# Kernel optimization log

Hardware: AMD Instinct MI355X
Metric: run time of the kernel (lower is better)

The kernel has to match this reference:

```python
import jax, jax.numpy as jnp
import numpy as np

K = 3  # unfold kernel size
K2 = K * K


def conv1x1_relu(x, w):
    # x: (B, C, H, W), w: (O, C)  -- BasicConv2d(channel, channel, 1, bias=False) + ReLU
    return jax.nn.relu(jnp.einsum('bchw,oc->bohw', x, w))


def unfold3x3(x, d=1):
    # torch nn.Unfold(kernel_size=3, padding=d, dilation=d): returns (B, C, 9, H, W)
    # with kernel index k = 3*i + j varying per channel block (channel-major, matching
    # the '(c k2)' split in the original rearrange).
    B, C, H, W = x.shape
    xp = jnp.pad(x, ((0, 0), (0, 0), (d, d), (d, d)))
    pats = [xp[:, :, i * d:i * d + H, j * d:j * d + W]
            for i in range(K) for j in range(K)]
    return jnp.stack(pats, axis=2)  # (B, C, 9, H, W)


def setup_inputs() -> dict:
    key = jax.random.key(0)
    k0, k1, k2, k3 = jax.random.split(key, 4)
    n, t, c, h, w = 2, 4, 64, 64, 96
    x = jax.random.normal(k0, (n, t, c, h, w), dtype=jnp.float32)
    # BasicConv2d inits conv weights with std=0.01
    w1 = jax.random.normal(k1, (c, c), dtype=jnp.float32) * 0.01
    w2 = jax.random.normal(k2, (c, c), dtype=jnp.float32) * 0.01
    w3 = jax.random.normal(k3, (c, c), dtype=jnp.float32) * 0.01
    return {'x': x, 'w1': w1, 'w2': w2, 'w3': w3}


def reference(x, w1, w2, w3):
    n, t, c, h, w = x.shape
    hw = h * w
    xf = x.reshape(n * t, c, h, w)

    x1 = unfold3x3(conv1x1_relu(xf, w1))  # (nt, c, 9, h, w)
    x2 = unfold3x3(conv1x1_relu(xf, w2))
    x3 = unfold3x3(conv1x1_relu(xf, w3))

    # x1: '(n t) (c k2) hw -> n hw t k2 c'
    x1 = x1.reshape(n, t, c, K2, hw).transpose(0, 4, 1, 3, 2)  # (n, hw, t, k2, c)
    x1_mean = jnp.mean(x1, axis=3)                              # (n, hw, t, c)
    x1_var = jnp.var(x1, axis=3, ddof=1)                        # unbiased
    x1f = x1.reshape(n, hw, t * K2, c)

    # x2: '(n t) (c k2) hw -> n hw c t k2'
    x2 = x2.reshape(n, t, c, K2, hw).transpose(0, 4, 2, 1, 3)   # (n, hw, c, t, k2)
    x2_mean = jnp.mean(x2, axis=4)                              # (n, hw, c, t)
    x2_var = jnp.var(x2, axis=4, ddof=1)
    x2f = x2.reshape(n, hw, c, t * K2)

    score1 = jax.nn.softmax(jnp.matmul(x1f, x2f), axis=-1)       # (n, hw, t*k2, t*k2)
    score2 = jax.nn.softmax(jnp.matmul(x1_var, x2_var), axis=-1) # (n, hw, t, t)
    score3 = jax.nn.softmax(jnp.matmul(x1_mean, x2_mean), axis=-1)

    # x3: '(n t) (c k2) hw -> n hw t (k2 c)'
    x3 = x3.reshape(n, t, c, K2, hw).transpose(0, 4, 1, 3, 2)   # (n, hw, t, k2, c)
    x3tk = x3.reshape(n, hw, t, K2 * c)
    x4 = jnp.matmul(score3, x3tk) + jnp.matmul(score2, x3tk)     # (n, hw, t, k2*c)
    x4 = x4.reshape(n, hw, t, K2, c)

    x3f = x3.reshape(n, hw, t * K2, c)
    x5 = jnp.matmul(score1, x3f).reshape(n, hw, t, K2, c)

    x6 = x5 + x4                                                 # (n, hw, t, k2, c)
    center = x6[:, :, :, K2 // 2, :][..., None]                  # (n, hw, t, c, 1)
    score4 = jax.nn.softmax(jnp.matmul(x6, center), axis=-2)     # (n, hw, t, k2, 1)
    out = jnp.sum(x6 * score4, axis=-2)                          # (n, hw, t, c)

    # 'n (h w) t c -> n t c h w'
    out = out.reshape(n, h, w, t, c).transpose(0, 3, 4, 1, 2)
    return out
```

## Files before the change

### kernel.cpp

```cpp
#include <hip/hip_runtime.h>

#define HW 6144
#define HH 64
#define WWID 96

typedef __attribute__((ext_vector_type(8))) _Float16 half8;
typedef __attribute__((ext_vector_type(2))) _Float16 half2v;
typedef __attribute__((ext_vector_type(8))) unsigned short ushort8;
typedef __attribute__((ext_vector_type(4))) float floatx4;
typedef __attribute__((ext_vector_type(4))) uint uint4v;
typedef __attribute__((ext_vector_type(4))) int int4v;

static __device__ __forceinline__ ushort f2h(float x) {
  _Float16 h = (_Float16)x;
  return __builtin_bit_cast(ushort, h);
}
static __device__ __forceinline__ float h2f(ushort b) {
  return (float)__builtin_bit_cast(_Float16, b);
}
static __device__ __forceinline__ uint pk2h(float a, float b) {
  return __builtin_bit_cast(uint, __builtin_amdgcn_cvt_pkrtz(a, b));
}
static __device__ __forceinline__ float hdot2(uint a, uint b, float c) {
#if __has_builtin(__builtin_amdgcn_fdot2)
  return __builtin_amdgcn_fdot2(__builtin_bit_cast(half2v, a),
                                __builtin_bit_cast(half2v, b), c, false);
#else
  c = fmaf(h2f((ushort)a), h2f((ushort)b), c);
  return fmaf(h2f((ushort)(a >> 16)), h2f((ushort)(b >> 16)), c);
#endif
}
static __device__ __forceinline__ half2v h2shfl16(half2v v) {
  return __builtin_bit_cast(half2v,
      (uint)__shfl_xor((int)__builtin_bit_cast(uint, v), 16));
}

__global__ __launch_bounds__(256) void conv_mfma_kernel(
    const float* __restrict__ X, const float* __restrict__ W1,
    const float* __restrict__ W2, const float* __restrict__ W3,
    ushort* __restrict__ Y1, ushort* __restrict__ Y2, ushort* __restrict__ Y3) {
  __shared__ __align__(16) ushort Xt[32 * 72];
  const int tid = threadIdx.x;
  const int wid = tid >> 6, lane = tid & 63;
  const int b = blockIdx.x / 192;
  const int p0 = (blockIdx.x % 192) * 32;

  if (blockIdx.x == 0 && tid < 96) {
    int which = tid >> 5, i = tid & 31;
    ushort* Ys = which == 0 ? Y1 : which == 1 ? Y2 : Y3;
    ((uint*)(Ys + (size_t)8 * HW * 64))[i] = 0u;
  }

#pragma unroll
  for (int it = 0; it < 2; ++it) {
    int idx = it * 256 + tid;
    int c = idx >> 3, pq = idx & 7;
    floatx4 v = *(const floatx4*)&X[((size_t)b * 64 + c) * HW + p0 + 4 * pq];
#pragma unroll
    for (int j = 0; j < 4; ++j) {
      int p = 4 * pq + j;
      Xt[p * 72 + (c ^ (p & 56))] = f2h(v[j]);
    }
  }
  __syncthreads();

  const int col = lane & 15, kg = lane >> 4;
  const int ph = wid & 1, mth = wid >> 1;
  const int p = ph * 16 + col;
  half8 b0 = *(const half8*)&Xt[p * 72 + ((kg * 8) ^ (p & 56))];
  half8 b1 = *(const half8*)&Xt[p * 72 + ((kg * 8 + 32) ^ (p & 56))];
  const size_t pixbase = ((size_t)b * HW + p0 + p) * 64;

  for (int s = 0; s < 3; ++s) {
    const float* Wf = (s == 0) ? W1 : (s == 1) ? W2 : W3;
    ushort* Y = (s == 0) ? Y1 : (s == 1) ? Y2 : Y3;
#pragma unroll
    for (int m = 0; m < 2; ++m) {
      int mt = mth * 2 + m;
      const float* wp = &Wf[(mt * 16 + col) * 64 + kg * 8];
      floatx4 w0 = *(const floatx4*)wp;
      floatx4 w1v = *(const floatx4*)(wp + 4);
      floatx4 w2v = *(const floatx4*)(wp + 32);
      floatx4 w3v = *(const floatx4*)(wp + 36);
      uint4v ua, ub;
      ua[0] = pk2h(w0[0], w0[1]);  ua[1] = pk2h(w0[2], w0[3]);
      ua[2] = pk2h(w1v[0], w1v[1]); ua[3] = pk2h(w1v[2], w1v[3]);
      ub[0] = pk2h(w2v[0], w2v[1]); ub[1] = pk2h(w2v[2], w2v[3]);
      ub[2] = pk2h(w3v[0], w3v[1]); ub[3] = pk2h(w3v[2], w3v[3]);
      half8 a0 = __builtin_bit_cast(half8, ua);
      half8 a1 = __builtin_bit_cast(half8, ub);
      floatx4 acc = {0.f, 0.f, 0.f, 0.f};
      acc = __builtin_amdgcn_mfma_f32_16x16x32_f16(a0, b0, acc, 0, 0, 0);
      acc = __builtin_amdgcn_mfma_f32_16x16x32_f16(a1, b1, acc, 0, 0, 0);
      uint2 u;
      u.x = pk2h(fmaxf(acc[0], 0.f), fmaxf(acc[1], 0.f));
      u.y = pk2h(fmaxf(acc[2], 0.f), fmaxf(acc[3], 0.f));
      *(uint2*)&Y[pixbase + mt * 16 + 4 * kg] = u;
    }
  }
}

__global__ __launch_bounds__(256, 7) void attn_kernel(
    const ushort* __restrict__ Y1, const ushort* __restrict__ Y2,
    const ushort* __restrict__ Y3, float* __restrict__ out) {
  __shared__ __align__(16) ushort XS[2 * 48 * 72];
  __shared__ __align__(16) ushort P1b[48 * 72];
  __shared__ __align__(16) uint mmv[2][128];
  __shared__ __align__(16) uint vvv[2][128];

  ushort* X1b = XS;
  ushort* X2b = XS + 48 * 72;
  float* X6f = (float*)XS;
  float* SSf = (float*)vvv;
  float* L4f = (float*)mmv;

  const int tid = threadIdx.x;
  const int wid = tid >> 6;
  const int lane = tid & 63;
  const int bid0 = blockIdx.x;
  const int bid = (bid0 & 7) * (12288 >> 3) + (bid0 >> 3);
  const int pix = bid % HW;
  const int nn = bid / HW;
  const int h = pix / WWID, w = pix - h * WWID;
  const int tb0 = nn * 4;
  const int SINKE = 8 * HW * 64;

  {
    const int s = wid >> 1;
    const int t = (wid & 1) * 2 + (lane >> 5);
    const int kh = (lane >> 4) & 1;
    const int cq = lane & 15;
    const ushort* Ysrc = s ? Y2 : Y1;
    const int base = (tb0 + t) * HW + pix;
    half2v s1a = {0, 0}, s1b = {0, 0}, s2a = {0, 0}, s2b = {0, 0};
#pragma unroll
    for (int i = 0; i < 5; ++i) {
      int k = 2 * i + kh;
      if (k < 9) {
        int k3 = (k * 11) >> 5;
        int dh = k3 - 1, dw = k - 3 * k3 - 1;
        bool valid = ((unsigned)(h + dh) < HH) & ((unsigned)(w + dw) < WWID);
        int off = valid ? (base + dh * WWID + dw) * 64 : SINKE;
        uint2 uv = *(const uint2*)&Ysrc[off + 4 * cq];
        *(uint2*)&XS[s * 3456 + (t * 9 + k) * 72 + 4 * cq] = uv;
        half2v va = __builtin_bit_cast(half2v, uv.x);
        half2v vb = __builtin_bit_cast(half2v, uv.y);
        s1a += va; s2a += va * va;
        s1b += vb; s2b += vb * vb;
      }
    }
    s1a += h2shfl16(s1a);
    s1b += h2shfl16(s1b);
    s2a += h2shfl16(s2a);
    s2b += h2shfl16(s2b);
    if (kh == 0) {
      float s1f[4] = {(float)s1a[0], (float)s1a[1], (float)s1b[0], (float)s1b[1]};
      float s2f[4] = {(float)s2a[0], (float)s2a[1], (float)s2b[0], (float)s2b[1]};
      float mf[4], vf[4];
#pragma unroll
      for (int j = 0; j < 4; ++j) {
        mf[j] = s1f[j] * (1.f / 9.f);
        vf[j] = (s2f[j] - s1f[j] * s1f[j] * (1.f / 9.f)) * 0.125f;
      }
      mmv[s][t * 32 + 2 * cq] = pk2h(mf[0], mf[1]);
      mmv[s][t * 32 + 2 * cq + 1] = pk2h(mf[2], mf[3]);
      vvv[s][t * 32 + 2 * cq] = pk2h(vf[0], vf[1]);
      vvv[s][t * 32 + 2 * cq + 1] = pk2h(vf[2], vf[3]);
    }
  }
  if (tid < 64) {
    int b = tid;
    int o = SINKE * 2;
    if (b < 36) {
      int t = (b * 57) >> 9;
      int k = b - 9 * t;
      int k3 = (k * 11) >> 5;
      int hh = h + k3 - 1, ww = w + (k - 3 * k3) - 1;
      if ((unsigned)hh < HH && (unsigned)ww < WWID)
        o = ((tb0 + t) * HW + hh * WWID + ww) * 128;
    }
    ((int*)&P1b[(b >> 2) * 72 + 64])[b & 3] = o;
  }
  for (int i = tid; i < 384; i += 256) {
    int r = i >> 3, u = i & 7;
    *(uint*)&P1b[r * 72 + 48 + 2 * u] = 0u;
  }
  for (int i = tid; i < 192; i += 256) {
    int r = i >> 4, cq = i & 15;
    uint2 z; z.x = 0u; z.y = 0u;
    *(uint2*)&X2b[(36 + r) * 72 + 4 * cq] = z;
  }
  __syncthreads();

  const int colL = lane & 15, kg = lane >> 4;
  ushort8 xv0, xv1;
  {
    const int c2 = (wid * 16 + colL) * 2;
    const char* Y3b = (const char*)Y3;
    int4v oa = *(const int4v*)&P1b[(kg * 2) * 72 + 64];
    int4v ob = *(const int4v*)&P1b[(kg * 2 + 1) * 72 + 64];
    int4v oc = *(const int4v*)&P1b[(kg * 2 + 8) * 72 + 64];
    int4v od = *(const int4v*)&P1b[(kg * 2 + 9) * 72 + 64];
#pragma unroll
    for (int j = 0; j < 4; ++j) {
      xv0[j] = *(const ushort*)(Y3b + (oa[j] + c2));
      xv0[4 + j] = *(const ushort*)(Y3b + (ob[j] + c2));
      xv1[j] = *(const ushort*)(Y3b + (oc[j] + c2));
      xv1[4 + j] = *(const ushort*)(Y3b + (od[j] + c2));
    }
  }

  if (wid < 3) {
    floatx4 ac0 = {0.f, 0.f, 0.f, 0.f}, ac1 = ac0, ac2 = ac0;
    int ar = (wid * 16 + colL) * 72 + (kg << 3);
    half8 a0 = *(const half8*)&X1b[ar];
    half8 a1 = *(const half8*)&X1b[ar + 32];
    int brb = colL * 72 + (kg << 3);
    ac0 = __builtin_amdgcn_mfma_f32_16x16x32_f16(a0, *(const half8*)&X2b[brb], ac0, 0, 0, 0);
    ac0 = __builtin_amdgcn_mfma_f32_16x16x32_f16(a1, *(const half8*)&X2b[brb + 32], ac0, 0, 0, 0);
    ac1 = __builtin_amdgcn_mfma_f32_16x16x32_f16(a0, *(const half8*)&X2b[brb + 16 * 72], ac1, 0, 0, 0);
    ac1 = __builtin_amdgcn_mfma_f32_16x16x32_f16(a1, *(const half8*)&X2b[brb + 16 * 72 + 32], ac1, 0, 0, 0);
    ac2 = __builtin_amdgcn_mfma_f32_16x16x32_f16(a0, *(const half8*)&X2b[brb + 32 * 72], ac2, 0, 0, 0);
    ac2 = __builtin_amdgcn_mfma_f32_16x16x32_f16(a1, *(const half8*)&X2b[brb + 32 * 72 + 32], ac2, 0, 0, 0);

    bool v2 = (colL < 4);
#pragma unroll
    for (int r = 0; r < 4; ++r) {
      float e0 = __expf(ac0[r]);
      float e1 = __expf(ac1[r]);
      float e2 = __expf(ac2[r]);
      float sm = e0 + e1 + (v2 ? e2 : 0.f);
#pragma unroll
      for (int d = 1; d < 16; d <<= 1) sm += __shfl_xor(sm, d);
      float rs = __builtin_amdgcn_rcpf(sm);
      int ro = (wid * 16 + 4 * kg + r) * 72 + colL;
      P1b[ro] = f2h(e0 * rs);
      P1b[ro + 16] = f2h(e1 * rs);
      P1b[ro + 32] = f2h(e2 * rs);
    }
  } else {
    int pr = lane >> 2, q = lane & 3;
    int t1 = pr >> 2, t2 = pr & 3;
    float a3 = 0.f, a2 = 0.f;
#pragma unroll
    for (int j = 0; j < 8; ++j) {
      int cp = q * 8 + j;
      a3 = hdot2(mmv[0][t1 * 32 + cp], mmv[1][t2 * 32 + cp], a3);
      a2 = hdot2(vvv[0][t1 * 32 + cp], vvv[1][t2 * 32 + cp], a2);
    }
    a3 += __shfl_xor(a3, 1);
    a3 += __shfl_xor(a3, 2);
    a2 += __shfl_xor(a2, 1);
    a2 += __shfl_xor(a2, 2);
    if (q == 0) { SSf[pr] = a3; SSf[16 + pr] = a2; }
    if (lane < 4) {
      floatx4 v3 = *(const floatx4*)&SSf[lane * 4];
      floatx4 v2v = *(const floatx4*)&SSf[16 + lane * 4];
      float e3[4], e2v[4], s3 = 0.f, s2v = 0.f;
#pragma unroll
      for (int j = 0; j < 4; ++j) {
        e3[j] = __expf(v3[j]); s3 += e3[j];
        e2v[j] = __expf(v2v[j]); s2v += e2v[j];
      }
      float r3 = __builtin_amdgcn_rcpf(s3), r2 = __builtin_amdgcn_rcpf(s2v);
      floatx4 mm;
#pragma unroll
      for (int j = 0; j < 4; ++j) mm[j] = fmaf(e3[j], r3, e2v[j] * r2);
      *(floatx4*)&SSf[32 + lane * 4] = mm;
    }
  }
  __syncthreads();

  if (tid < 144) {
    int a = tid >> 2, t2i = tid & 3;
    int ta = (a * 57) >> 9;
    int ka = a - 9 * ta;
    int off = a * 72 + t2i * 9 + ka;
    P1b[off] = f2h(h2f(P1b[off]) + SSf[32 + ta * 4 + t2i]);
  }
  __syncthreads();

  {
    half8 xb0 = __builtin_bit_cast(half8, xv0);
    half8 xb1 = __builtin_bit_cast(half8, xv1);
    int c = wid * 16 + colL;
#pragma unroll
    for (int ti = 0; ti < 3; ++ti) {
      floatx4 acc = {0.f, 0.f, 0.f, 0.f};
      int ar = (ti * 16 + colL) * 72 + (kg << 3);
      acc = __builtin_amdgcn_mfma_f32_16x16x32_f16(*(const half8*)&P1b[ar], xb0, acc, 0, 0, 0);
      acc = __builtin_amdgcn_mfma_f32_16x16x32_f16(*(const half8*)&P1b[ar + 32], xb1, acc, 0, 0, 0);
      int r0 = ti * 16 + (kg << 2);
#pragma unroll
      for (int r = 0; r < 4; ++r) {
        int a = r0 + r;
        if (a < 36) X6f[a * 68 + c] = acc[r];
      }
    }
  }
  __syncthreads();

  if (tid < 144) {
    int a = tid >> 2, q = tid & 3;
    int ctr = ((a * 57) >> 9) * 9 + 4;
    const floatx4* rowA = (const floatx4*)&X6f[a * 68 + q * 16];
    const floatx4* rowC = (const floatx4*)&X6f[ctr * 68 + q * 16];
    float s = 0.f;
#pragma unroll
    for (int j = 0; j < 4; ++j) {
      floatx4 va = rowA[j], vc = rowC[j];
      s = fmaf(va[0], vc[0], s);
      s = fmaf(va[1], vc[1], s);
      s = fmaf(va[2], vc[2], s);
      s = fmaf(va[3], vc[3], s);
    }
    s += __shfl_xor(s, 1);
    s += __shfl_xor(s, 2);
    if (q == 0) L4f[a] = __expf(s);
  }
  __syncthreads();

  {
    float den = 0.f, num = 0.f;
#pragma unroll
    for (int k = 0; k < 9; ++k) {
      float e = L4f[wid * 9 + k];
      den += e;
      num = fmaf(X6f[(wid * 9 + k) * 68 + lane], e, num);
    }
    out[((size_t)(tb0 + wid) * 64 + lane) * HW + pix] = num * __builtin_amdgcn_rcpf(den);
  }
}

extern "C" void kernel_launch(void* const* d_in, const int* in_sizes, int n_in,
                              void* d_out, int out_size, void* d_ws, size_t ws_size,
                              hipStream_t stream) {
  const float* x = (const float*)d_in[0];
  const float* w1 = (const float*)d_in[1];
  const float* w2 = (const float*)d_in[2];
  const float* w3 = (const float*)d_in[3];
  float* out = (float*)d_out;

  size_t ysz = (size_t)8 * HW * 64;
  size_t ypitch = ysz + 64;
  ushort* Y1 = (ushort*)d_ws;
  ushort* Y2 = Y1 + ypitch;
  ushort* Y3 = Y2 + ypitch;

  conv_mfma_kernel<<<dim3(1536), dim3(256), 0, stream>>>(x, w1, w2, w3, Y1, Y2, Y3);
  attn_kernel<<<dim3(2 * HW), dim3(256), 0, stream>>>(Y1, Y2, Y3, out);
}
```

Before: 73.62 us.

## Pack attention shared memory into one compact buffer to fit eight blocks per CU

Replaces the separate shared arrays with a single packed buffer in which X1 takes 36 rows instead of 48 and P1 rows beyond 36 are no longer stored. This reduces LDS per block so that launch bounds can request eight resident blocks instead of seven. The cost is extra bounds checks on the P1 writes and tighter offset arithmetic, with a risk of overlap between regions (X2 starts at 2592 yet zero-pads rows 36..47).

```diff
diff --git a/kernel.cpp b/kernel.cpp
--- a/kernel.cpp
+++ b/kernel.cpp
@@ -100,17 +100,17 @@
   }
 }
 
-__global__ __launch_bounds__(256, 7) void attn_kernel(
+__global__ __launch_bounds__(256, 8) void attn_kernel(
     const ushort* __restrict__ Y1, const ushort* __restrict__ Y2,
     const ushort* __restrict__ Y3, float* __restrict__ out) {
-  __shared__ __align__(16) ushort XS[2 * 48 * 72];
-  __shared__ __align__(16) ushort P1b[48 * 72];
-  __shared__ __align__(16) uint mmv[2][128];
-  __shared__ __align__(16) uint vvv[2][128];
-
-  ushort* X1b = XS;
-  ushort* X2b = XS + 48 * 72;
-  float* X6f = (float*)XS;
+  __shared__ __align__(16) ushort SMEM[9664];
+
+  ushort* X1b = SMEM;
+  ushort* X2b = SMEM + 2592;
+  ushort* P1b = SMEM + 6048;
+  uint* mmv = (uint*)(SMEM + 8640);
+  uint* vvv = (uint*)(SMEM + 9152);
+  float* X6f = (float*)SMEM;
   float* SSf = (float*)vvv;
   float* L4f = (float*)mmv;
 
@@ -142,7 +142,7 @@
         bool valid = ((unsigned)(h + dh) < HH) & ((unsigned)(w + dw) < WWID);
         int off = valid ? (base + dh * WWID + dw) * 64 : SINKE;
         uint2 uv = *(const uint2*)&Ysrc[off + 4 * cq];
-        *(uint2*)&XS[s * 3456 + (t * 9 + k) * 72 + 4 * cq] = uv;
+        *(uint2*)&SMEM[s * 2592 + (t * 9 + k) * 72 + 4 * cq] = uv;
         half2v va = __builtin_bit_cast(half2v, uv.x);
         half2v vb = __builtin_bit_cast(half2v, uv.y);
         s1a += va; s2a += va * va;
@@ -162,10 +162,10 @@
         mf[j] = s1f[j] * (1.f / 9.f);
         vf[j] = (s2f[j] - s1f[j] * s1f[j] * (1.f / 9.f)) * 0.125f;
       }
-      mmv[s][t * 32 + 2 * cq] = pk2h(mf[0], mf[1]);
-      mmv[s][t * 32 + 2 * cq + 1] = pk2h(mf[2], mf[3]);
-      vvv[s][t * 32 + 2 * cq] = pk2h(vf[0], vf[1]);
-      vvv[s][t * 32 + 2 * cq + 1] = pk2h(vf[2], vf[3]);
+      mmv[s * 128 + t * 32 + 2 * cq] = pk2h(mf[0], mf[1]);
+      mmv[s * 128 + t * 32 + 2 * cq + 1] = pk2h(mf[2], mf[3]);
+      vvv[s * 128 + t * 32 + 2 * cq] = pk2h(vf[0], vf[1]);
+      vvv[s * 128 + t * 32 + 2 * cq + 1] = pk2h(vf[2], vf[3]);
     }
   }
   if (tid < 64) {
@@ -181,7 +181,7 @@
     }
     ((int*)&P1b[(b >> 2) * 72 + 64])[b & 3] = o;
   }
-  for (int i = tid; i < 384; i += 256) {
+  for (int i = tid; i < 288; i += 256) {
     int r = i >> 3, u = i & 7;
     *(uint*)&P1b[r * 72 + 48 + 2 * u] = 0u;
   }
@@ -233,10 +233,13 @@
 #pragma unroll
       for (int d = 1; d < 16; d <<= 1) sm += __shfl_xor(sm, d);
       float rs = __builtin_amdgcn_rcpf(sm);
-      int ro = (wid * 16 + 4 * kg + r) * 72 + colL;
-      P1b[ro] = f2h(e0 * rs);
-      P1b[ro + 16] = f2h(e1 * rs);
-      P1b[ro + 32] = f2h(e2 * rs);
+      int row = wid * 16 + 4 * kg + r;
+      if (row < 36) {
+        int ro = row * 72 + colL;
+        P1b[ro] = f2h(e0 * rs);
+        P1b[ro + 16] = f2h(e1 * rs);
+        P1b[ro + 32] = f2h(e2 * rs);
+      }
     }
   } else {
     int pr = lane >> 2, q = lane & 3;
@@ -245,8 +248,8 @@
 #pragma unroll
     for (int j = 0; j < 8; ++j) {
       int cp = q * 8 + j;
-      a3 = hdot2(mmv[0][t1 * 32 + cp], mmv[1][t2 * 32 + cp], a3);
-      a2 = hdot2(vvv[0][t1 * 32 + cp], vvv[1][t2 * 32 + cp], a2);
+      a3 = hdot2(mmv[t1 * 32 + cp], mmv[128 + t2 * 32 + cp], a3);
+      a2 = hdot2(vvv[t1 * 32 + cp], vvv[128 + t2 * 32 + cp], a2);
     }
     a3 += __shfl_xor(a3, 1);
     a3 += __shfl_xor(a3, 2);
```

Result: no change. 73.07 us (-0.8%).
